# Kernel tuning notes

Measured on AMD Instinct MI355X. Metric: run time of the kernel, lower is better.

The kernel has to match this reference:

```python
import jax, jax.numpy as jnp
import numpy as np

B, H, W, C = 16, 56, 56, 512
P = 7           # partition (window) size
NH, DH = 16, 32 # n_heads, head_dim (NH*DH == C)
EPS = 1e-6      # flax nnx LayerNorm default epsilon

def _rel_index(size):
    coords = np.stack(np.meshgrid(np.arange(size), np.arange(size), indexing='ij')).reshape(2, -1)
    rel = coords[:, :, None] - coords[:, None, :]
    rh = rel[0] + (size - 1)
    rw = rel[1] + (size - 1)
    return jnp.asarray(rh * (2 * size - 1) + rw)  # [P*P, P*P] int

REL_IDX = _rel_index(P)

def setup_inputs() -> dict:
    key = jax.random.key(0)
    ks = jax.random.split(key, 6)
    s = lambda k, shape: jax.random.normal(k, shape, jnp.float32) * 0.02
    return {
        'x': jax.random.normal(ks[0], (B, H, W, C), jnp.float32),
        'ln1_s': jnp.ones((C,), jnp.float32), 'ln1_b': jnp.zeros((C,), jnp.float32),
        'w_qkv': s(ks[1], (C, 3 * C)), 'b_qkv': jnp.zeros((3 * C,), jnp.float32),
        'bias_table': s(ks[2], ((2 * P - 1) ** 2, NH)),
        'w_merge': s(ks[3], (C, C)), 'b_merge': jnp.zeros((C,), jnp.float32),
        'ln2_s': jnp.ones((C,), jnp.float32), 'ln2_b': jnp.zeros((C,), jnp.float32),
        'w1': s(ks[4], (C, 4 * C)), 'b1': jnp.zeros((4 * C,), jnp.float32),
        'w2': s(ks[5], (4 * C, C)), 'b2': jnp.zeros((C,), jnp.float32),
    }

def _ln(x, s, b):
    m = x.mean(-1, keepdims=True)
    v = ((x - m) ** 2).mean(-1, keepdims=True)
    return (x - m) * jax.lax.rsqrt(v + EPS) * s + b

def reference(x, ln1_s, ln1_b, w_qkv, b_qkv, bias_table, w_merge, b_merge,
              ln2_s, ln2_b, w1, b1, w2, b2):
    Bn, Hh, Ww, Cc = x.shape
    HP, WP = Hh // P, Ww // P
    # window partition: [B,H,W,C] -> [B, G=HP*WP, P*P, C]
    xp = x.reshape(Bn, HP, P, WP, P, Cc).transpose(0, 1, 3, 2, 4, 5).reshape(Bn, HP * WP, P * P, Cc)
    # --- attention block (pre-LN) ---
    h = _ln(xp, ln1_s, ln1_b)
    qkv = h @ w_qkv + b_qkv
    q, k, v = jnp.split(qkv, 3, axis=-1)
    heads = lambda t: t.reshape(Bn, HP * WP, P * P, NH, DH).transpose(0, 1, 3, 2, 4)
    q = heads(q)
    k = heads(k) * (Cc ** -0.5)  # module scales by feat_dim**-0.5 (faithful)
    v = heads(v)
    # relative position bias gather: [NH, P*P, P*P]
    bias = bias_table[REL_IDX.reshape(-1)].reshape(P * P, P * P, NH).transpose(2, 0, 1)
    scores = jnp.einsum('bghid,bghjd->bghij', q, k) + bias
    attn = jax.nn.softmax(scores, axis=-1)
    o = jnp.einsum('bghij,bghjd->bghid', attn, v)
    o = o.transpose(0, 1, 3, 2, 4).reshape(Bn, HP * WP, P * P, Cc)
    xp = xp + (o @ w_merge + b_merge)
    # --- MLP block (pre-LN) ---
    m = _ln(xp, ln2_s, ln2_b)
    xp = xp + (jax.nn.gelu(m @ w1 + b1) @ w2 + b2)
    # window departition: [B, G, P*P, C] -> [B, H, W, C]
    return xp.reshape(Bn, HP, WP, P, P, Cc).transpose(0, 1, 3, 2, 4, 5).reshape(Bn, Hh, Ww, Cc)
```

## Files before the change

### kernel.cpp

```cpp
#include <hip/hip_runtime.h>
#include <stdint.h>

typedef unsigned short u16;
typedef u16    u16x8  __attribute__((ext_vector_type(8)));
typedef __bf16 bf16x8 __attribute__((ext_vector_type(8)));
typedef float  f32x4  __attribute__((ext_vector_type(4)));

#define TOKS 50176
#define CD   512

__device__ __forceinline__ float bf2f(u16 u) {
    union { unsigned int i; float f; } c; c.i = ((unsigned int)u) << 16; return c.f;
}
__device__ __forceinline__ u16 f2bf(float f) {
    union { float f; unsigned int i; } c; c.f = f;
    unsigned int x = c.i;
    return (u16)((x + 0x7fffu + ((x >> 16) & 1u)) >> 16);
}
__device__ __forceinline__ float gelu_tanh(float x) {
    float t = 0.7978845608028654f * (x + 0.044715f * x * x * x);
    float e = __expf(2.0f * t);
    float th = 1.0f - 2.0f / (e + 1.0f);
    return 0.5f * x * (1.0f + th);
}

__global__ __launch_bounds__(256)
void k_transpose_cast(const float* __restrict__ src, u16* __restrict__ dst,
                      const int K, const int N)
{
    __shared__ float tile[32][33];
    const int tx = threadIdx.x & 31, ty = threadIdx.x >> 5;
    const int n0 = blockIdx.x * 32, k0 = blockIdx.y * 32;
    #pragma unroll
    for (int i = 0; i < 4; ++i) {
        int r = ty + i * 8;
        tile[r][tx] = src[(size_t)(k0 + r) * N + n0 + tx];
    }
    __syncthreads();
    #pragma unroll
    for (int i = 0; i < 4; ++i) {
        int r = ty + i * 8;
        dst[(size_t)(n0 + r) * K + k0 + tx] = f2bf(tile[tx][r]);
    }
}

__global__ __launch_bounds__(256)
void k_layernorm(const float* __restrict__ x, const float* __restrict__ g,
                 const float* __restrict__ bvec, u16* __restrict__ out)
{
    const int l = threadIdx.x & 63;
    const int w = threadIdx.x >> 6;
    const size_t row = (size_t)blockIdx.x * 4 + w;
    const float* xr = x + row * CD + l * 8;
    f32x4 v0 = *(const f32x4*)xr;
    f32x4 v1 = *(const f32x4*)(xr + 4);
    float s = 0.f, sq = 0.f;
    #pragma unroll
    for (int i = 0; i < 4; ++i) { s += v0[i]; sq += v0[i] * v0[i]; }
    #pragma unroll
    for (int i = 0; i < 4; ++i) { s += v1[i]; sq += v1[i] * v1[i]; }
    #pragma unroll
    for (int off = 32; off > 0; off >>= 1) {
        s  += __shfl_xor(s, off);
        sq += __shfl_xor(sq, off);
    }
    const float mean = s * (1.0f / 512.0f);
    const float var  = fmaxf(sq * (1.0f / 512.0f) - mean * mean, 0.0f);
    const float rstd = rsqrtf(var + 1e-6f);
    const int c = l * 8;
    f32x4 g0 = *(const f32x4*)(g + c),    g1 = *(const f32x4*)(g + c + 4);
    f32x4 b0 = *(const f32x4*)(bvec + c), b1 = *(const f32x4*)(bvec + c + 4);
    u16x8 o;
    #pragma unroll
    for (int i = 0; i < 4; ++i) o[i]     = f2bf((v0[i] - mean) * rstd * g0[i] + b0[i]);
    #pragma unroll
    for (int i = 0; i < 4; ++i) o[4 + i] = f2bf((v1[i] - mean) * rstd * g1[i] + b1[i]);
    *(u16x8*)(out + row * CD + c) = o;
}

template<int EPI>
__global__ __launch_bounds__(256)
void k_gemm(const u16* __restrict__ A, const u16* __restrict__ Bt,
            const float* __restrict__ bias, const float* __restrict__ resid,
            u16* __restrict__ outb, float* __restrict__ outf,
            const int N, const int K)
{
    __shared__ u16 As[128 * 32];
    __shared__ u16 Bs[128 * 32];
    const int t  = threadIdx.x;
    const int l  = t & 63;
    const int w  = t >> 6;
    const int wr = w >> 1, wc = w & 1;
    const int m0 = blockIdx.x * 128, n0 = blockIdx.y * 128;
    const int sr = t >> 2;
    const int sq = t & 3;
    const int kq = l >> 4;
    const int fr = l & 15;

    const u16* Ap0 = A  + (size_t)(m0 + sr) * K      + sq * 8;
    const u16* Ap1 = A  + (size_t)(m0 + 64 + sr) * K + sq * 8;
    const u16* Bp0 = Bt + (size_t)(n0 + sr) * K      + sq * 8;
    const u16* Bp1 = Bt + (size_t)(n0 + 64 + sr) * K + sq * 8;
    const int wo0 = sr * 32 + sq * 8;
    const int wo1 = (64 + sr) * 32 + sq * 8;

    f32x4 acc[4][4];
    #pragma unroll
    for (int i = 0; i < 4; ++i)
        #pragma unroll
        for (int j = 0; j < 4; ++j) {
            f32x4 z = {0.f, 0.f, 0.f, 0.f};
            acc[i][j] = z;
        }

    for (int k0 = 0; k0 < K; k0 += 32) {
        u16x8 a0 = *(const u16x8*)(Ap0 + k0);
        u16x8 a1 = *(const u16x8*)(Ap1 + k0);
        u16x8 b0 = *(const u16x8*)(Bp0 + k0);
        u16x8 b1 = *(const u16x8*)(Bp1 + k0);
        __syncthreads();
        *(u16x8*)&As[wo0] = a0;
        *(u16x8*)&As[wo1] = a1;
        *(u16x8*)&Bs[wo0] = b0;
        *(u16x8*)&Bs[wo1] = b1;
        __syncthreads();
        bf16x8 af[4], bfv[4];
        #pragma unroll
        for (int mi = 0; mi < 4; ++mi)
            af[mi] = *(const bf16x8*)&As[(wr * 64 + mi * 16 + fr) * 32 + kq * 8];
        #pragma unroll
        for (int ni = 0; ni < 4; ++ni)
            bfv[ni] = *(const bf16x8*)&Bs[(wc * 64 + ni * 16 + fr) * 32 + kq * 8];
        #pragma unroll
        for (int mi = 0; mi < 4; ++mi)
            #pragma unroll
            for (int ni = 0; ni < 4; ++ni)
                acc[mi][ni] = __builtin_amdgcn_mfma_f32_16x16x32_bf16(
                    af[mi], bfv[ni], acc[mi][ni], 0, 0, 0);
    }

    float bv[4];
    #pragma unroll
    for (int ni = 0; ni < 4; ++ni) bv[ni] = bias[n0 + wc * 64 + ni * 16 + fr];

    #pragma unroll
    for (int mi = 0; mi < 4; ++mi) {
        #pragma unroll
        for (int r = 0; r < 4; ++r) {
            const size_t row  = (size_t)(m0 + wr * 64 + mi * 16 + kq * 4 + r);
            const size_t base = row * N + n0 + wc * 64 + fr;
            #pragma unroll
            for (int ni = 0; ni < 4; ++ni) {
                float v = acc[mi][ni][r] + bv[ni];
                if (EPI == 1) v = gelu_tanh(v);
                if (EPI == 2) outf[base + ni * 16] = v + resid[base + ni * 16];
                else          outb[base + ni * 16] = f2bf(v);
            }
        }
    }
}

__global__ __launch_bounds__(64)
void k_attn(const u16* __restrict__ qkv, const float* __restrict__ btab,
            u16* __restrict__ o, const int tok_base)
{
    __shared__ float Ss[64 * 53];
    const int l    = threadIdx.x;
    const int widl = blockIdx.x >> 4;
    const int head = blockIdx.x & 15;
    const int bl   = widl >> 6;
    const int g    = widl & 63;
    const int gh   = g >> 3, gw = g & 7;
    const int tok00 = bl * 3136 + gh * 392 + gw * 7;
    const int pl = (l < 49) ? l : 48;
    const int ph = pl / 7, pw = pl - (pl / 7) * 7;
    const int tokl = tok00 + ph * 56 + pw;

    float q[32];
    {
        const size_t qoff = (size_t)tokl * 1536 + head * 32;
        #pragma unroll
        for (int i = 0; i < 4; ++i) {
            u16x8 u = *(const u16x8*)(qkv + qoff + i * 8);
            #pragma unroll
            for (int j = 0; j < 8; ++j) q[i * 8 + j] = bf2f(u[j]);
        }
    }

    float rowmax = -1e30f;
    {
        int j = 0;
        for (int jh = 0; jh < 7; ++jh) {
            for (int jw = 0; jw < 7; ++jw, ++j) {
                const size_t koff = (size_t)(tok00 + jh * 56 + jw) * 1536 + 512 + head * 32;
                float d0 = 0.f, d1 = 0.f, d2 = 0.f, d3 = 0.f;
                #pragma unroll
                for (int i = 0; i < 4; ++i) {
                    u16x8 u = *(const u16x8*)(qkv + koff + i * 8);
                    d0 += q[i * 8 + 0] * bf2f(u[0]); d0 += q[i * 8 + 1] * bf2f(u[1]);
                    d1 += q[i * 8 + 2] * bf2f(u[2]); d1 += q[i * 8 + 3] * bf2f(u[3]);
                    d2 += q[i * 8 + 4] * bf2f(u[4]); d2 += q[i * 8 + 5] * bf2f(u[5]);
                    d3 += q[i * 8 + 6] * bf2f(u[6]); d3 += q[i * 8 + 7] * bf2f(u[7]);
                }
                const float bias = btab[(size_t)((ph - jh + 6) * 13 + (pw - jw + 6)) * 16 + head];
                const float sc = (d0 + d1 + d2 + d3) * 0.04419417382415922f + bias;
                rowmax = fmaxf(rowmax, sc);
                Ss[l * 53 + j] = sc;
            }
        }
    }

    float sum = 0.f;
    for (int j = 0; j < 49; ++j) {
        float p = __expf(Ss[l * 53 + j] - rowmax);
        sum += p;
        Ss[l * 53 + j] = p;
    }

    float oa[32];
    #pragma unroll
    for (int i = 0; i < 32; ++i) oa[i] = 0.f;
    {
        int j = 0;
        for (int jh = 0; jh < 7; ++jh) {
            for (int jw = 0; jw < 7; ++jw, ++j) {
                const size_t voff = (size_t)(tok00 + jh * 56 + jw) * 1536 + 1024 + head * 32;
                const float p = Ss[l * 53 + j];
                #pragma unroll
                for (int i = 0; i < 4; ++i) {
                    u16x8 u = *(const u16x8*)(qkv + voff + i * 8);
                    #pragma unroll
                    for (int jj = 0; jj < 8; ++jj) oa[i * 8 + jj] += p * bf2f(u[jj]);
                }
            }
        }
    }

    if (l < 49) {
        const float inv = 1.0f / sum;
        const size_t obase = (size_t)(tok_base + tokl) * CD + head * 32;
        #pragma unroll
        for (int i = 0; i < 4; ++i) {
            u16x8 u;
            #pragma unroll
            for (int jj = 0; jj < 8; ++jj) u[jj] = f2bf(oa[i * 8 + jj] * inv);
            *(u16x8*)(o + obase + i * 8) = u;
        }
    }
}

extern "C" void kernel_launch(void* const* d_in, const int* in_sizes, int n_in,
                              void* d_out, int out_size, void* d_ws, size_t ws_size,
                              hipStream_t stream)
{
    (void)in_sizes; (void)n_in; (void)out_size; (void)ws_size;
    const float* x     = (const float*)d_in[0];
    const float* ln1_s = (const float*)d_in[1];
    const float* ln1_b = (const float*)d_in[2];
    const float* w_qkv = (const float*)d_in[3];
    const float* b_qkv = (const float*)d_in[4];
    const float* btab  = (const float*)d_in[5];
    const float* w_mrg = (const float*)d_in[6];
    const float* b_mrg = (const float*)d_in[7];
    const float* ln2_s = (const float*)d_in[8];
    const float* ln2_b = (const float*)d_in[9];
    const float* w1    = (const float*)d_in[10];
    const float* b1    = (const float*)d_in[11];
    const float* w2    = (const float*)d_in[12];
    const float* b2    = (const float*)d_in[13];
    float* out = (float*)d_out;

    u16* wqkvT = (u16*)d_ws;
    u16* wmrgT = wqkvT + (size_t)1536 * 512;
    u16* w1T   = wmrgT + (size_t)512 * 512;
    u16* w2T   = w1T   + (size_t)2048 * 512;
    u16* hbuf  = w2T   + (size_t)512 * 2048;
    u16* mbuf  = hbuf  + (size_t)TOKS * 512;
    float* y1  = (float*)(mbuf + (size_t)TOKS * 512);
    u16* qkvc  = (u16*)(y1 + (size_t)TOKS * 512);
    u16* hidc  = qkvc + (size_t)6272 * 1536;

    dim3 B256(256);

    k_transpose_cast<<<dim3(48, 16), B256, 0, stream>>>(w_qkv, wqkvT, 512, 1536);
    k_transpose_cast<<<dim3(16, 16), B256, 0, stream>>>(w_mrg, wmrgT, 512, 512);
    k_transpose_cast<<<dim3(64, 16), B256, 0, stream>>>(w1,   w1T,   512, 2048);
    k_transpose_cast<<<dim3(16, 64), B256, 0, stream>>>(w2,   w2T,   2048, 512);

    k_layernorm<<<dim3(TOKS / 4), B256, 0, stream>>>(x, ln1_s, ln1_b, hbuf);

    for (int c = 0; c < 8; ++c) {
        const size_t tb = (size_t)c * 6272;
        k_gemm<0><<<dim3(49, 12), B256, 0, stream>>>(
            hbuf + tb * 512, wqkvT, b_qkv, nullptr, qkvc, nullptr, 1536, 512);
        k_attn<<<dim3(128 * 16), dim3(64), 0, stream>>>(qkvc, btab, hbuf, (int)tb);
    }

    k_gemm<2><<<dim3(392, 4), B256, 0, stream>>>(
        hbuf, wmrgT, b_mrg, x, nullptr, y1, 512, 512);

    k_layernorm<<<dim3(TOKS / 4), B256, 0, stream>>>(y1, ln2_s, ln2_b, mbuf);

    for (int c = 0; c < 2; ++c) {
        const size_t rb = (size_t)c * 25088;
        k_gemm<1><<<dim3(196, 16), B256, 0, stream>>>(
            mbuf + rb * 512, w1T, b1, nullptr, hidc, nullptr, 2048, 512);
        k_gemm<2><<<dim3(196, 4), B256, 0, stream>>>(
            hidc, w2T, b2, y1 + rb * 512, nullptr, out + rb * 512, 512, 2048);
    }
}
```

Before: 1.239 ms.

## Load GEMM tiles directly to LDS with XOR swizzle and swap grid order

The GEMM tile loads now use global_load_lds, which writes global data straight into shared memory without passing through registers. A lane permutation and an XOR swizzle of the LDS layout are added to cut bank conflicts on the fragment reads. The grid axes are swapped so that consecutive blocks walk along N and share the same A rows, which should improve cache reuse. A full vmcnt(0) wait still runs each iteration with no double buffering, so global latency remains exposed.

Measured after the change: 1.247 ms. Within noise of the previous version (+0.6%).

```diff
diff --git a/kernel.cpp b/kernel.cpp
--- a/kernel.cpp
+++ b/kernel.cpp
@@ -22,6 +22,12 @@
     float e = __expf(2.0f * t);
     float th = 1.0f - 2.0f / (e + 1.0f);
     return 0.5f * x * (1.0f + th);
+}
+
+typedef const __attribute__((address_space(1))) unsigned int gas_u32;
+typedef __attribute__((address_space(3))) unsigned int las_u32;
+__device__ __forceinline__ void gload16(const u16* g, u16* l) {
+    __builtin_amdgcn_global_load_lds((gas_u32*)g, (las_u32*)l, 16, 0, 0);
 }
 
 __global__ __launch_bounds__(256)
@@ -91,18 +97,33 @@
     const int l  = t & 63;
     const int w  = t >> 6;
     const int wr = w >> 1, wc = w & 1;
-    const int m0 = blockIdx.x * 128, n0 = blockIdx.y * 128;
-    const int sr = t >> 2;
-    const int sq = t & 3;
+    const int m0 = blockIdx.y * 128, n0 = blockIdx.x * 128;
     const int kq = l >> 4;
     const int fr = l & 15;
 
-    const u16* Ap0 = A  + (size_t)(m0 + sr) * K      + sq * 8;
-    const u16* Ap1 = A  + (size_t)(m0 + 64 + sr) * K + sq * 8;
-    const u16* Bp0 = Bt + (size_t)(n0 + sr) * K      + sq * 8;
-    const u16* Bp1 = Bt + (size_t)(n0 + 64 + sr) * K + sq * 8;
-    const int wo0 = sr * 32 + sq * 8;
-    const int wo1 = (64 + sr) * 32 + sq * 8;
+    const int lam  = t ^ ((t >> 3) & 7);
+    const int srow = lam >> 2;
+    const int skq  = lam & 3;
+    const u16* Asrc0 = A  + (size_t)(m0 + srow) * K      + skq * 8;
+    const u16* Asrc1 = A  + (size_t)(m0 + 64 + srow) * K + skq * 8;
+    const u16* Bsrc0 = Bt + (size_t)(n0 + srow) * K      + skq * 8;
+    const u16* Bsrc1 = Bt + (size_t)(n0 + 64 + srow) * K + skq * 8;
+    u16* Adst0 = As + w * 512;
+    u16* Adst1 = As + 2048 + w * 512;
+    u16* Bdst0 = Bs + w * 512;
+    u16* Bdst1 = Bs + 2048 + w * 512;
+
+    int offA[4], offB[4];
+    #pragma unroll
+    for (int mi = 0; mi < 4; ++mi) {
+        int lr = (wr * 64 + mi * 16 + fr) * 4 + kq;
+        offA[mi] = (lr ^ ((lr >> 3) & 7)) * 8;
+    }
+    #pragma unroll
+    for (int ni = 0; ni < 4; ++ni) {
+        int lr = (wc * 64 + ni * 16 + fr) * 4 + kq;
+        offB[ni] = (lr ^ ((lr >> 3) & 7)) * 8;
+    }
 
     f32x4 acc[4][4];
     #pragma unroll
@@ -114,23 +135,18 @@
         }
 
     for (int k0 = 0; k0 < K; k0 += 32) {
-        u16x8 a0 = *(const u16x8*)(Ap0 + k0);
-        u16x8 a1 = *(const u16x8*)(Ap1 + k0);
-        u16x8 b0 = *(const u16x8*)(Bp0 + k0);
-        u16x8 b1 = *(const u16x8*)(Bp1 + k0);
         __syncthreads();
-        *(u16x8*)&As[wo0] = a0;
-        *(u16x8*)&As[wo1] = a1;
-        *(u16x8*)&Bs[wo0] = b0;
-        *(u16x8*)&Bs[wo1] = b1;
+        gload16(Asrc0 + k0, Adst0);
+        gload16(Asrc1 + k0, Adst1);
+        gload16(Bsrc0 + k0, Bdst0);
+        gload16(Bsrc1 + k0, Bdst1);
+        asm volatile("s_waitcnt vmcnt(0)" ::: "memory");
         __syncthreads();
         bf16x8 af[4], bfv[4];
         #pragma unroll
-        for (int mi = 0; mi < 4; ++mi)
-            af[mi] = *(const bf16x8*)&As[(wr * 64 + mi * 16 + fr) * 32 + kq * 8];
-        #pragma unroll
-        for (int ni = 0; ni < 4; ++ni)
-            bfv[ni] = *(const bf16x8*)&Bs[(wc * 64 + ni * 16 + fr) * 32 + kq * 8];
+        for (int mi = 0; mi < 4; ++mi) af[mi]  = *(const bf16x8*)&As[offA[mi]];
+        #pragma unroll
+        for (int ni = 0; ni < 4; ++ni) bfv[ni] = *(const bf16x8*)&Bs[offB[ni]];
         #pragma unroll
         for (int mi = 0; mi < 4; ++mi)
             #pragma unroll
@@ -291,21 +307,21 @@
 
     for (int c = 0; c < 8; ++c) {
         const size_t tb = (size_t)c * 6272;
-        k_gemm<0><<<dim3(49, 12), B256, 0, stream>>>(
+        k_gemm<0><<<dim3(12, 49), B256, 0, stream>>>(
             hbuf + tb * 512, wqkvT, b_qkv, nullptr, qkvc, nullptr, 1536, 512);
         k_attn<<<dim3(128 * 16), dim3(64), 0, stream>>>(qkvc, btab, hbuf, (int)tb);
     }
 
-    k_gemm<2><<<dim3(392, 4), B256, 0, stream>>>(
+    k_gemm<2><<<dim3(4, 392), B256, 0, stream>>>(
         hbuf, wmrgT, b_mrg, x, nullptr, y1, 512, 512);
 
     k_layernorm<<<dim3(TOKS / 4), B256, 0, stream>>>(y1, ln2_s, ln2_b, mbuf);
 
     for (int c = 0; c < 2; ++c) {
         const size_t rb = (size_t)c * 25088;
-        k_gemm<1><<<dim3(196, 16), B256, 0, stream>>>(
+        k_gemm<1><<<dim3(16, 196), B256, 0, stream>>>(
             mbuf + rb * 512, w1T, b1, nullptr, hidc, nullptr, 2048, 512);
-        k_gemm<2><<<dim3(196, 4), B256, 0, stream>>>(
+        k_gemm<2><<<dim3(4, 196), B256, 0, stream>>>(
             hidc, w2T, b2, y1 + rb * 512, nullptr, out + rb * 512, 512, 2048);
     }
 }
```
